# Kernel tuning notes

Hardware: AMD Instinct MI355X
Metric: run time of the kernel (lower is better)

## Reference

```python
import jax, jax.numpy as jnp
import numpy as np

B, SI, ST, D = 2, 1024, 512, 2048
H, KV, HD = 16, 4, 128
E, F, TOPK = 8, 1024, 2
EPS = 1e-6


def _rms(x, w):
    x32 = x.astype(jnp.float32)
    y = x32 * jax.lax.rsqrt(jnp.mean(x32 * x32, axis=-1, keepdims=True) + EPS)
    return y.astype(x.dtype) * w


def _rope(x, cos, sin):
    # x: [B,S,h,HD]; cos/sin: [S,HD//2]. Complex-pair rotation (use_real=False path):
    # pairs (x[2i], x[2i+1]) treated as complex, multiplied by e^{i theta}.
    xr, xi = x[..., 0::2], x[..., 1::2]
    c = cos[None, :, None, :]
    s = sin[None, :, None, :]
    out_r = xr * c - xi * s
    out_i = xr * s + xi * c
    return jnp.stack([out_r, out_i], axis=-1).reshape(x.shape)


def setup_inputs() -> dict:
    key = jax.random.key(0)
    ks = jax.random.split(key, 12)
    def w(k, shape, fan_in):
        return jax.random.normal(k, shape, jnp.float32) * (fan_in ** -0.5)
    pos_i = np.arange(SI)[:, None].astype(np.float32)
    pos_t = np.arange(ST)[:, None].astype(np.float32)
    inv = (1.0 / (10000.0 ** (np.arange(0, HD, 2).astype(np.float32) / HD)))[None, :]
    return {
        'hidden_states': jax.random.normal(ks[0], (B, SI, D), jnp.float32),
        'encoder_hidden_states': jax.random.normal(ks[1], (B, ST, D), jnp.float32),
        'img_cos': jnp.asarray(np.cos(pos_i * inv), jnp.float32),
        'img_sin': jnp.asarray(np.sin(pos_i * inv), jnp.float32),
        'txt_cos': jnp.asarray(np.cos(pos_t * inv), jnp.float32),
        'txt_sin': jnp.asarray(np.sin(pos_t * inv), jnp.float32),
        'norm1_w': jnp.ones((D,), jnp.float32),
        'norm2_w': jnp.ones((D,), jnp.float32),
        'wq': w(ks[2], (D, H * HD), D),
        'wk': w(ks[3], (D, KV * HD), D),
        'wv': w(ks[4], (D, KV * HD), D),
        'wk_txt': w(ks[5], (D, KV * HD), D),
        'wv_txt': w(ks[6], (D, KV * HD), D),
        'wo': w(ks[7], (H * HD, D), H * HD),
        'q_norm_w': jnp.ones((HD,), jnp.float32),
        'k_norm_w': jnp.ones((HD,), jnp.float32),
        'added_k_norm_w': jnp.ones((HD,), jnp.float32),
        'router_w': w(ks[8], (D, E), D),
        'gate_up_proj': w(ks[9], (E, D, 2 * F), D),
        'down_proj': w(ks[10], (E, F, D), F),
    }


def reference(hidden_states, encoder_hidden_states, img_cos, img_sin, txt_cos, txt_sin,
              norm1_w, norm2_w, wq, wk, wv, wk_txt, wv_txt, wo,
              q_norm_w, k_norm_w, added_k_norm_w, router_w, gate_up_proj, down_proj):
    h = hidden_states
    # ---- cross-attn: image queries over concat(image, text) K/V, GQA + RoPE ----
    x = _rms(h, norm1_w)
    q = _rms((x @ wq).reshape(B, SI, H, HD), q_norm_w)
    k_img = _rms((x @ wk).reshape(B, SI, KV, HD), k_norm_w)
    v_img = (x @ wv).reshape(B, SI, KV, HD)
    q = _rope(q, img_cos, img_sin)
    k_img = _rope(k_img, img_cos, img_sin)
    k_txt = _rms((encoder_hidden_states @ wk_txt).reshape(B, ST, KV, HD), added_k_norm_w)
    k_txt = _rope(k_txt, txt_cos, txt_sin)
    v_txt = (encoder_hidden_states @ wv_txt).reshape(B, ST, KV, HD)
    k = jnp.concatenate([k_img, k_txt], axis=1)  # [B, SI+ST, KV, HD]
    v = jnp.concatenate([v_img, v_txt], axis=1)
    k = jnp.repeat(k, H // KV, axis=2)  # GQA repeat_interleave over heads
    v = jnp.repeat(v, H // KV, axis=2)
    scores = jnp.einsum('bqhd,bkhd->bhqk', q, k) * (HD ** -0.5)
    attn = jax.nn.softmax(scores.astype(jnp.float32), axis=-1).astype(q.dtype)
    o = jnp.einsum('bhqk,bkhd->bqhd', attn, v).reshape(B, SI, H * HD)
    h = h + o @ wo
    # ---- MoE: top-k router + packed SwiGLU experts ----
    xt = _rms(h, norm2_w).reshape(B * SI, D)
    probs = jax.nn.softmax((xt @ router_w).astype(jnp.float32), axis=-1)
    topv, topi = jax.lax.top_k(probs, TOPK)
    topv = topv / jnp.sum(topv, axis=-1, keepdims=True)
    wgt = jnp.sum(jax.nn.one_hot(topi, E, dtype=xt.dtype) * topv.astype(xt.dtype)[..., None], axis=1)  # [T,E]
    gate_up = jnp.einsum('td,edg->teg', xt, gate_up_proj)  # [T,E,2F]
    gate, up = gate_up[..., :F], gate_up[..., F:]
    act = jax.nn.silu(gate) * up
    eo = jnp.einsum('tef,efd->ted', act, down_proj)  # [T,E,D]
    moe_out = jnp.einsum('te,ted->td', wgt, eo).reshape(B, SI, D)
    return h + moe_out
```

## Files before the change

kernel.cpp:

```cpp
#include <hip/hip_runtime.h>


typedef __attribute__((ext_vector_type(8))) __bf16 bf16x8;
typedef __attribute__((ext_vector_type(8))) unsigned short u16x8;
typedef __attribute__((ext_vector_type(4))) unsigned short u16x4;
typedef __attribute__((ext_vector_type(4))) float f32x4;

__device__ __forceinline__ unsigned short f2bf(float x) {
  unsigned u = __builtin_bit_cast(unsigned, x);
  u += 0x7fffu + ((u >> 16) & 1u);
  return (unsigned short)(u >> 16);
}
__device__ __forceinline__ float bf2f(unsigned short b) {
  return __builtin_bit_cast(float, ((unsigned)b) << 16);
}

__device__ __forceinline__ void glds16(const unsigned short* g, unsigned short* l) {
  __builtin_amdgcn_global_load_lds(
      (const __attribute__((address_space(1))) void*)g,
      (__attribute__((address_space(3))) void*)l, 16, 0, 0);
}

__device__ __forceinline__ int xcd_swz(int orig, int nwg) {
  int q = nwg >> 3, r = nwg & 7;
  int xcd = orig & 7, idx = orig >> 3;
  int base = (xcd < r) ? xcd * (q + 1) : r * (q + 1) + (xcd - r) * q;
  return base + idx;
}

struct CvtJobs {
  const float* src[8];
  unsigned short* dst[8];
  int K[8];
  int N[8];
  int off[9];
};

__global__ __launch_bounds__(256) void convert_all(CvtJobs jb)
{
  __shared__ unsigned short T[64][66];
  const int bid = blockIdx.x;
  int j = 0;
  #pragma unroll
  for (int i = 0; i < 8; ++i) if (bid >= jb.off[i + 1]) j = i + 1;
  const int local = bid - jb.off[j];
  const int K = jb.K[j], N = jb.N[j];
  const int kb = K >> 6, nb = N >> 6;
  const int kt = local % kb;
  const int rest = local / kb;
  const int nt = rest % nb, zi = rest / nb;
  const float* Wz = jb.src[j] + (size_t)zi * K * N;
  unsigned short* WTz = jb.dst[j] + (size_t)zi * K * N;
  const int k0 = kt * 64, n0 = nt * 64;
  const int tid = threadIdx.x;
  #pragma unroll
  for (int i = tid; i < 64 * 16; i += 256) {
    int k = i >> 4, n4 = (i & 15) * 4;
    float4 v = *(const float4*)&Wz[(size_t)(k0 + k) * N + n0 + n4];
    T[n4 + 0][k] = f2bf(v.x);
    T[n4 + 1][k] = f2bf(v.y);
    T[n4 + 2][k] = f2bf(v.z);
    T[n4 + 3][k] = f2bf(v.w);
  }
  __syncthreads();
  #pragma unroll
  for (int i = tid; i < 64 * 8; i += 256) {
    int n = i >> 3, k8 = (i & 7) * 8;
    *(u16x8*)&WTz[(size_t)(n0 + n) * K + k0 + k8] = *(const u16x8*)&T[n][k8];
  }
}

struct Epi {
  unsigned short* qb;
  unsigned short* kbuf;
  unsigned short* vbuf;
  const float* q_nw;
  const float* k_nw;
  const float* kt_nw;
  const float* icos;
  const float* isin;
  const float* tcos;
  const float* tsin;
  float scale;
};

__global__ __launch_bounds__(256) void gemm_bb(
    const unsigned short* __restrict__ A, const unsigned short* __restrict__ BT,
    float* __restrict__ C, const float* __restrict__ resid,
    int M, int N, int K, int mode, Epi ep)
{
  __shared__ unsigned short As[2][128 * 64];
  __shared__ unsigned short Bs[2][128 * 64];
  const int mb = M >> 7;
  const int w = xcd_swz(blockIdx.x, gridDim.x);
  const int bm = (w % mb) * 128, bn = (w / mb) * 128;
  const int tid = threadIdx.x, lane = tid & 63, wid = tid >> 6;
  const int wm = (wid >> 1) * 64, wn = (wid & 1) * 64;
  const int l16 = lane & 15, g4 = lane >> 4;
  const int rseg = lane >> 3;
  const int csw  = ((lane & 7) ^ rseg) * 8;
  const unsigned short* aSrc[4];
  const unsigned short* bSrc[4];
  #pragma unroll
  for (int p = 0; p < 4; ++p) {
    int row = (p * 4 + wid) * 8 + rseg;
    aSrc[p] = A  + (size_t)(bm + row) * K + csw;
    bSrc[p] = BT + (size_t)(bn + row) * K + csw;
  }
  f32x4 acc[4][4] = {};
  const int NT = K >> 6;
  #pragma unroll
  for (int p = 0; p < 4; ++p) glds16(aSrc[p], &As[0][(p * 4 + wid) * 512]);
  #pragma unroll
  for (int p = 0; p < 4; ++p) glds16(bSrc[p], &Bs[0][(p * 4 + wid) * 512]);
  for (int t = 0; t < NT; ++t) {
    const int cur = t & 1;
    if (t + 1 < NT) {
      const int k0 = (t + 1) << 6;
      #pragma unroll
      for (int p = 0; p < 4; ++p) glds16(aSrc[p] + k0, &As[cur ^ 1][(p * 4 + wid) * 512]);
      #pragma unroll
      for (int p = 0; p < 4; ++p) glds16(bSrc[p] + k0, &Bs[cur ^ 1][(p * 4 + wid) * 512]);
      asm volatile("s_waitcnt vmcnt(8)" ::: "memory");
    } else {
      asm volatile("s_waitcnt vmcnt(0)" ::: "memory");
    }
    __builtin_amdgcn_s_barrier();
    __builtin_amdgcn_sched_barrier(0);
    const unsigned short* ab = &As[cur][0];
    const unsigned short* bb = &Bs[cur][0];
    #pragma unroll
    for (int ks = 0; ks < 2; ++ks) {
      bf16x8 af[4], bf[4];
      #pragma unroll
      for (int i = 0; i < 4; ++i) {
        int ra = wm + i * 16 + l16;
        int rb = wn + i * 16 + l16;
        int ch = ((ks * 4 + g4) ^ (l16 & 7)) * 8;
        af[i] = *(const bf16x8*)&ab[ra * 64 + ch];
        bf[i] = *(const bf16x8*)&bb[rb * 64 + ch];
      }
      #pragma unroll
      for (int mi = 0; mi < 4; ++mi)
        #pragma unroll
        for (int ni = 0; ni < 4; ++ni)
          acc[mi][ni] = __builtin_amdgcn_mfma_f32_16x16x32_bf16(af[mi], bf[ni], acc[mi][ni], 0, 0, 0);
    }
    __builtin_amdgcn_sched_barrier(0);
    __builtin_amdgcn_s_barrier();
  }
  const int r4 = g4 * 4;

  if (mode == 0) {
    #pragma unroll
    for (int mi = 0; mi < 4; ++mi)
      #pragma unroll
      for (int ni = 0; ni < 4; ++ni)
        #pragma unroll
        for (int r = 0; r < 4; ++r) {
          int row = bm + wm + mi * 16 + r4 + r;
          int col = bn + wn + ni * 16 + l16;
          float v = acc[mi][ni][r];
          if (resid) v += resid[(size_t)row * N + col];
          C[(size_t)row * N + col] = v;
        }
    return;
  }

  const int bt = bn >> 7;
  unsigned short* dst;
  const float* nw = nullptr;
  const float* cosT = nullptr;
  const float* sinT = nullptr;
  int h, NH, st, soff, vkind = 0, shift;
  float premul = 1.f;
  int S;
  if (mode == 1) {
    S = 1024; shift = 10;
    if (bt < 16)      { h = bt;      dst = ep.qb;   nw = ep.q_nw; cosT = ep.icos; sinT = ep.isin;
                        NH = 16; st = 1024; soff = 0; premul = ep.scale; }
    else if (bt < 20) { h = bt - 16; dst = ep.kbuf; nw = ep.k_nw; cosT = ep.icos; sinT = ep.isin;
                        NH = 4;  st = 1536; soff = 0; }
    else              { h = bt - 20; dst = ep.vbuf; vkind = 1; NH = 4; st = 1536; soff = 0; }
  } else {
    S = 512; shift = 9;
    if (bt < 4) { h = bt;     dst = ep.kbuf; nw = ep.kt_nw; cosT = ep.tcos; sinT = ep.tsin;
                  NH = 4; st = 1536; soff = 1024; }
    else        { h = bt - 4; dst = ep.vbuf; vkind = 1; NH = 4; st = 1536; soff = 1024; }
  }

  if (vkind) {
    #pragma unroll
    for (int mi = 0; mi < 4; ++mi)
      #pragma unroll
      for (int ni = 0; ni < 4; ++ni)
        #pragma unroll
        for (int r = 0; r < 4; ++r) {
          int row = wm + mi * 16 + r4 + r;
          int d   = wn + ni * 16 + l16;
          int token = bm + row;
          int srow = token & (S - 1), bidx = token >> shift;
          dst[((size_t)(bidx * NH + h) * st + srow + soff) * 128 + d] = f2bf(acc[mi][ni][r]);
        }
    return;
  }

  float* ssb = (float*)&As[0][0];
  float ssp[4][4];
  #pragma unroll
  for (int mi = 0; mi < 4; ++mi)
    #pragma unroll
    for (int r = 0; r < 4; ++r) {
      float v = 0.f;
      #pragma unroll
      for (int ni = 0; ni < 4; ++ni) v += acc[mi][ni][r] * acc[mi][ni][r];
      #pragma unroll
      for (int off = 1; off < 16; off <<= 1) v += __shfl_xor(v, off);
      ssp[mi][r] = v;
    }
  __syncthreads();
  if (l16 == 0) {
    #pragma unroll
    for (int mi = 0; mi < 4; ++mi)
      #pragma unroll
      for (int r = 0; r < 4; ++r)
        ssb[(wid & 1) * 128 + wm + mi * 16 + r4 + r] = ssp[mi][r];
  }
  __syncthreads();
  #pragma unroll
  for (int mi = 0; mi < 4; ++mi)
    #pragma unroll
    for (int r = 0; r < 4; ++r) {
      int row = wm + mi * 16 + r4 + r;
      float tot = ssb[row] + ssb[128 + row];
      float inv = rsqrtf(tot * (1.f / 128.f) + 1e-6f);
      int token = bm + row;
      int srow = token & (S - 1), bidx = token >> shift;
      #pragma unroll
      for (int ni = 0; ni < 4; ++ni) {
        int d = wn + ni * 16 + l16;
        float y = acc[mi][ni][r] * inv * nw[d];
        float part = __shfl_xor(y, 1);
        float c  = cosT[srow * 64 + (d >> 1)];
        float sn = sinT[srow * 64 + (d >> 1)];
        float outv = (d & 1) ? (part * sn + y * c) : (y * c - part * sn);
        dst[((size_t)(bidx * NH + h) * st + srow + soff) * 128 + d] = f2bf(outv * premul);
      }
    }
}

__global__ __launch_bounds__(512, 1) void gemm_moe_256sk(
    const unsigned short* __restrict__ A, const unsigned short* __restrict__ BTall,
    unsigned short* __restrict__ C0, unsigned short* __restrict__ C1,
    const int* __restrict__ counts, const int* __restrict__ offsets,
    const int* __restrict__ pair_token, const unsigned short* __restrict__ zbuf,
    int gather, int K, int N)
{
  const int w = xcd_swz(blockIdx.x, gridDim.x);
  const int e = w >> 7;
  const int local = w & 127;
  const int bm = ((local >> 4) & 7) * 256;
  const int kh = (local >> 3) & 1;
  const int bn = (local & 7) * 256;
  const int cnt = counts[e];
  if (bm >= cnt) return;
  const int base = offsets[e];
  const int Kh = K >> 1;
  unsigned short* __restrict__ C = kh ? C1 : C0;
  __shared__ unsigned short As[2][256 * 64];
  __shared__ unsigned short Bs[2][256 * 64];
  __shared__ int rowmap[256];
  const int tid = threadIdx.x, lane = tid & 63, wid = tid >> 6;
  const int wr = wid >> 2, wc = wid & 3;
  const int l16 = lane & 15, g4 = lane >> 4;
  const int rseg = lane >> 3;
  const int csw  = ((lane & 7) ^ rseg) * 8;
  if (tid < 256) {
    int lr = bm + tid;
    rowmap[tid] = (lr < cnt) ? (gather ? pair_token[base + lr] : base + lr) : -1;
  }
  __syncthreads();
  const unsigned short* BT = BTall + (size_t)e * N * K;
  const unsigned short* aSrc[4];
  const unsigned short* bSrc[4];
  int aOk[4];
  #pragma unroll
  for (int p = 0; p < 4; ++p) {
    int row = (p * 8 + wid) * 8 + rseg;
    int tok = rowmap[row];
    aOk[p] = (tok >= 0);
    aSrc[p] = aOk[p] ? (A + (size_t)tok * K + kh * Kh + csw) : (zbuf + csw);
    bSrc[p] = BT + (size_t)(bn + row) * K + kh * Kh + csw;
  }
  f32x4 acc[8][4] = {};
  const int NT = Kh >> 6;
  #pragma unroll
  for (int p = 0; p < 4; ++p) glds16(aSrc[p], &As[0][(p * 8 + wid) * 512]);
  #pragma unroll
  for (int p = 0; p < 4; ++p) glds16(bSrc[p], &Bs[0][(p * 8 + wid) * 512]);
  for (int t = 0; t < NT; ++t) {
    const int cur = t & 1;
    if (t + 1 < NT) {
      const int k0 = (t + 1) << 6;
      #pragma unroll
      for (int p = 0; p < 4; ++p)
        glds16(aSrc[p] + (aOk[p] ? k0 : 0), &As[cur ^ 1][(p * 8 + wid) * 512]);
      #pragma unroll
      for (int p = 0; p < 4; ++p)
        glds16(bSrc[p] + k0, &Bs[cur ^ 1][(p * 8 + wid) * 512]);
      asm volatile("s_waitcnt vmcnt(8)" ::: "memory");
    } else {
      asm volatile("s_waitcnt vmcnt(0)" ::: "memory");
    }
    __builtin_amdgcn_s_barrier();
    __builtin_amdgcn_sched_barrier(0);
    const unsigned short* ab = &As[cur][0];
    const unsigned short* bb = &Bs[cur][0];
    #pragma unroll
    for (int ks = 0; ks < 2; ++ks) {
      const int ch = ((ks * 4 + g4) ^ (l16 & 7)) * 8;
      bf16x8 bf[4];
      #pragma unroll
      for (int j = 0; j < 4; ++j)
        bf[j] = *(const bf16x8*)&bb[(wc * 64 + j * 16 + l16) * 64 + ch];
      #pragma unroll
      for (int mi = 0; mi < 8; ++mi) {
        bf16x8 af = *(const bf16x8*)&ab[(wr * 128 + mi * 16 + l16) * 64 + ch];
        #pragma unroll
        for (int ni = 0; ni < 4; ++ni)
          acc[mi][ni] = __builtin_amdgcn_mfma_f32_16x16x32_bf16(af, bf[ni], acc[mi][ni], 0, 0, 0);
      }
    }
    __builtin_amdgcn_sched_barrier(0);
    __builtin_amdgcn_s_barrier();
  }
  const int r4 = g4 * 4;
  #pragma unroll
  for (int mi = 0; mi < 8; ++mi)
    #pragma unroll
    for (int ni = 0; ni < 4; ++ni)
      #pragma unroll
      for (int r = 0; r < 4; ++r) {
        int lrow = bm + wr * 128 + mi * 16 + r4 + r;
        int col  = bn + wc * 64 + ni * 16 + l16;
        if (lrow < cnt)
          C[(size_t)(base + lrow) * N + col] = f2bf(acc[mi][ni][r]);
      }
}

__global__ __launch_bounds__(256) void pre_norm(
    const float* __restrict__ hidden, const float* __restrict__ w,
    unsigned short* __restrict__ x_bf,
    const float* __restrict__ enc, unsigned short* __restrict__ enc_bf)
{
  const int row = blockIdx.x;
  const int tid = threadIdx.x;
  if (row >= 2048) {
    const int r = row - 2048;
    const float* x = enc + (size_t)r * 2048 + tid * 8;
    unsigned short* o = enc_bf + (size_t)r * 2048 + tid * 8;
    float4 a = *(const float4*)&x[0];
    float4 b = *(const float4*)&x[4];
    o[0] = f2bf(a.x); o[1] = f2bf(a.y); o[2] = f2bf(a.z); o[3] = f2bf(a.w);
    o[4] = f2bf(b.x); o[5] = f2bf(b.y); o[6] = f2bf(b.z); o[7] = f2bf(b.w);
    return;
  }
  const float* x = hidden + (size_t)row * 2048;
  float4 a = *(const float4*)&x[tid * 8];
  float4 b = *(const float4*)&x[tid * 8 + 4];
  float s = a.x*a.x + a.y*a.y + a.z*a.z + a.w*a.w
          + b.x*b.x + b.y*b.y + b.z*b.z + b.w*b.w;
  #pragma unroll
  for (int off = 1; off < 64; off <<= 1) s += __shfl_xor(s, off);
  __shared__ float red[4];
  if ((tid & 63) == 0) red[tid >> 6] = s;
  __syncthreads();
  float inv = rsqrtf((red[0] + red[1] + red[2] + red[3]) * (1.f / 2048.f) + 1e-6f);
  float4 wa = *(const float4*)&w[tid * 8];
  float4 wb = *(const float4*)&w[tid * 8 + 4];
  unsigned short* o = x_bf + (size_t)row * 2048 + tid * 8;
  o[0] = f2bf(a.x * inv * wa.x); o[1] = f2bf(a.y * inv * wa.y);
  o[2] = f2bf(a.z * inv * wa.z); o[3] = f2bf(a.w * inv * wa.w);
  o[4] = f2bf(b.x * inv * wb.x); o[5] = f2bf(b.y * inv * wb.y);
  o[6] = f2bf(b.z * inv * wb.z); o[7] = f2bf(b.w * inv * wb.w);
}

__global__ __launch_bounds__(256) void rmsnorm_router(
    const float* __restrict__ in, const float* __restrict__ w,
    unsigned short* __restrict__ xt, const float* __restrict__ rw,
    int* __restrict__ topi, float* __restrict__ topw, int* __restrict__ counts)
{
  const int row = blockIdx.x;
  const int tid = threadIdx.x, lane = tid & 63, wid = tid >> 6;
  const float* x = in + (size_t)row * 2048;
  float4 a = *(const float4*)&x[tid * 8];
  float4 b = *(const float4*)&x[tid * 8 + 4];
  float s = a.x*a.x + a.y*a.y + a.z*a.z + a.w*a.w
          + b.x*b.x + b.y*b.y + b.z*b.z + b.w*b.w;
  #pragma unroll
  for (int off = 1; off < 64; off <<= 1) s += __shfl_xor(s, off);
  __shared__ float red[4];
  __shared__ float rl[4][8];
  if (lane == 0) red[wid] = s;
  __syncthreads();
  float inv = rsqrtf((red[0] + red[1] + red[2] + red[3]) * (1.f / 2048.f) + 1e-6f);
  float4 wa = *(const float4*)&w[tid * 8];
  float4 wb = *(const float4*)&w[tid * 8 + 4];
  float y[8] = {a.x * inv * wa.x, a.y * inv * wa.y, a.z * inv * wa.z, a.w * inv * wa.w,
                b.x * inv * wb.x, b.y * inv * wb.y, b.z * inv * wb.z, b.w * inv * wb.w};
  unsigned short* o = xt + (size_t)row * 2048 + tid * 8;
  #pragma unroll
  for (int j = 0; j < 8; ++j) o[j] = f2bf(y[j]);
  float lg[8] = {};
  #pragma unroll
  for (int j = 0; j < 8; ++j) {
    int d = tid * 8 + j;
    const float4 r0 = *(const float4*)&rw[d * 8];
    const float4 r1 = *(const float4*)&rw[d * 8 + 4];
    lg[0] += y[j] * r0.x; lg[1] += y[j] * r0.y; lg[2] += y[j] * r0.z; lg[3] += y[j] * r0.w;
    lg[4] += y[j] * r1.x; lg[5] += y[j] * r1.y; lg[6] += y[j] * r1.z; lg[7] += y[j] * r1.w;
  }
  #pragma unroll
  for (int e = 0; e < 8; ++e)
    #pragma unroll
    for (int off = 1; off < 64; off <<= 1) lg[e] += __shfl_xor(lg[e], off);
  if (lane == 0) {
    #pragma unroll
    for (int e = 0; e < 8; ++e) rl[wid][e] = lg[e];
  }
  __syncthreads();
  if (tid == 0) {
    float l[8];
    #pragma unroll
    for (int e = 0; e < 8; ++e) l[e] = rl[0][e] + rl[1][e] + rl[2][e] + rl[3][e];
    float v0 = l[0]; int e0 = 0;
    #pragma unroll
    for (int e = 1; e < 8; ++e) if (l[e] > v0) { v0 = l[e]; e0 = e; }
    float v1 = -1e30f; int e1 = 0;
    #pragma unroll
    for (int e = 0; e < 8; ++e) if (e != e0 && l[e] > v1) { v1 = l[e]; e1 = e; }
    float x1 = expf(v1 - v0);
    float w0 = 1.f / (1.f + x1);
    float w1 = x1 / (1.f + x1);
    topi[2 * row] = e0; topi[2 * row + 1] = e1;
    topw[2 * row] = w0; topw[2 * row + 1] = w1;
    atomicAdd(&counts[e0], 1);
    atomicAdd(&counts[e1], 1);
  }
}

__global__ __launch_bounds__(256) void route_build(
    const int* __restrict__ counts, int* __restrict__ offsets,
    const int* __restrict__ topi,
    int* __restrict__ pair_token, int* __restrict__ token_slot)
{
  __shared__ int soff[9];
  __shared__ int sfill[8];
  const int tid = threadIdx.x;
  if (tid == 0) {
    int a = 0;
    #pragma unroll
    for (int e = 0; e < 8; ++e) { soff[e] = a; a += counts[e]; }
    soff[8] = a;
  }
  if (tid < 8) sfill[tid] = 0;
  __syncthreads();
  if (tid < 9) offsets[tid] = soff[tid];
  for (int t = tid; t < 2048; t += 256) {
    #pragma unroll
    for (int k = 0; k < 2; ++k) {
      int e = topi[2 * t + k];
      int slot = soff[e] + atomicAdd(&sfill[e], 1);
      pair_token[slot] = t;
      token_slot[2 * t + k] = slot;
    }
  }
}

__global__ __launch_bounds__(512) void attn_kernel(
    const unsigned short* __restrict__ q,
    const unsigned short* __restrict__ kbuf,
    const unsigned short* __restrict__ vbuf,
    unsigned short* __restrict__ o)
{
  const int SK = 1536;
  const int w = xcd_swz(blockIdx.x, gridDim.x);
  const int bh = w >> 3;
  const int b = bh >> 4, h = bh & 15, kvh = h >> 2;
  const int q0 = (w & 7) * 128;
  const int tid = threadIdx.x, lane = tid & 63, wid = tid >> 6;
  const int l16 = lane & 15, kb = (lane >> 4) * 8, r4 = (lane >> 4) * 4;
  __shared__ unsigned short KsL[64 * 128];
  __shared__ unsigned short VTL[128 * 64];
  __shared__ unsigned short PsL[8 * 16 * 64];
  const int sr0 = tid >> 4;
  const int scc = (tid & 15) * 8;

  const unsigned short* qrow =
      q + ((size_t)(b * 16 + h) * 1024 + q0 + wid * 16 + l16) * 128;
  bf16x8 qf[4];
  #pragma unroll
  for (int ks = 0; ks < 4; ++ks) qf[ks] = *(const bf16x8*)&qrow[ks * 32 + kb];
  float mrow[4] = {-1e30f, -1e30f, -1e30f, -1e30f};
  float lrow[4] = {0.f, 0.f, 0.f, 0.f};
  f32x4 oacc[8] = {};
  const unsigned short* kb_base = kbuf + (size_t)(b * 4 + kvh) * SK * 128;
  const unsigned short* vb_base = vbuf + (size_t)(b * 4 + kvh) * SK * 128;

  u16x8 k0[2], v0[2], k1[2], v1[2];

#define ATT_LOAD(kr, vr, kt1)                                                 \
  {                                                                           \
    _Pragma("unroll")                                                         \
    for (int i = 0; i < 2; ++i) {                                             \
      kr[i] = *(const u16x8*)&kb_base[(size_t)((kt1) + sr0 + 32 * i) * 128 + scc]; \
      vr[i] = *(const u16x8*)&vb_base[(size_t)((kt1) + sr0 + 32 * i) * 128 + scc]; \
    }                                                                         \
  }

#define ATT_STAGE(kr, vr)                                                     \
  {                                                                           \
    _Pragma("unroll")                                                         \
    for (int i = 0; i < 2; ++i) {                                             \
      int rr = sr0 + 32 * i;                                                  \
      *(u16x8*)&KsL[rr * 128 + (((scc >> 3) ^ (rr & 7)) << 3)] = kr[i];       \
      _Pragma("unroll")                                                       \
      for (int j = 0; j < 8; ++j)                                             \
        VTL[(scc + j) * 64 + ((((rr >> 3) ^ ((scc + j) >> 3)) & 7) << 3) + (rr & 7)] = vr[i][j]; \
    }                                                                         \
  }

  auto compute = [&]() {
    f32x4 sacc[4] = {};
    __builtin_amdgcn_s_setprio(1);
    #pragma unroll
    for (int ks = 0; ks < 4; ++ks) {
      #pragma unroll
      for (int ni = 0; ni < 4; ++ni) {
        int rr = ni * 16 + l16;
        bf16x8 kf = *(const bf16x8*)
            &KsL[rr * 128 + ((((ks * 32 + kb) >> 3) ^ (rr & 7)) << 3)];
        sacc[ni] = __builtin_amdgcn_mfma_f32_16x16x32_bf16(qf[ks], kf, sacc[ni], 0, 0, 0);
      }
    }
    __builtin_amdgcn_s_setprio(0);
    float pv[4][4], alpha[4];
    #pragma unroll
    for (int r = 0; r < 4; ++r) {
      float tm = fmaxf(fmaxf(sacc[0][r], sacc[1][r]), fmaxf(sacc[2][r], sacc[3][r]));
      #pragma unroll
      for (int off = 1; off < 16; off <<= 1) tm = fmaxf(tm, __shfl_xor(tm, off));
      float mn = fmaxf(mrow[r], tm);
      alpha[r] = __expf(mrow[r] - mn);
      float s = 0.f;
      #pragma unroll
      for (int ni = 0; ni < 4; ++ni) {
        float p = __expf(sacc[ni][r] - mn);
        pv[ni][r] = p; s += p;
      }
      #pragma unroll
      for (int off = 1; off < 16; off <<= 1) s += __shfl_xor(s, off);
      lrow[r] = lrow[r] * alpha[r] + s;
      mrow[r] = mn;
    }
    #pragma unroll
    for (int ni = 0; ni < 8; ++ni)
      #pragma unroll
      for (int r = 0; r < 4; ++r) oacc[ni][r] *= alpha[r];
    #pragma unroll
    for (int ni = 0; ni < 4; ++ni)
      #pragma unroll
      for (int r = 0; r < 4; ++r) {
        int row = r4 + r, col = ni * 16 + l16;
        PsL[wid * 1024 + row * 64 + ((((col >> 3) ^ (row & 7)) & 7) << 3) + (col & 7)]
            = f2bf(pv[ni][r]);
      }
    asm volatile("s_waitcnt lgkmcnt(0)" ::: "memory");
    __builtin_amdgcn_sched_barrier(0);
    __builtin_amdgcn_s_setprio(1);
    #pragma unroll
    for (int ks = 0; ks < 2; ++ks) {
      bf16x8 pf = *(const bf16x8*)
          &PsL[wid * 1024 + l16 * 64 + ((((ks * 32 + kb) >> 3) ^ (l16 & 7)) << 3)];
      #pragma unroll
      for (int ni = 0; ni < 8; ++ni) {
        int d = ni * 16 + l16;
        bf16x8 vf = *(const bf16x8*)
            &VTL[d * 64 + ((((ks * 32 + kb) >> 3) ^ ((d >> 3) & 7)) << 3)];
        oacc[ni] = __builtin_amdgcn_mfma_f32_16x16x32_bf16(pf, vf, oacc[ni], 0, 0, 0);
      }
    }
    __builtin_amdgcn_s_setprio(0);
  };

  ATT_LOAD(k0, v0, 0);
  for (int t = 0; t < 24; t += 2) {
    ATT_STAGE(k0, v0);
    ATT_LOAD(k1, v1, (t + 1) * 64);
    asm volatile("s_waitcnt lgkmcnt(0)" ::: "memory");
    __builtin_amdgcn_s_barrier();
    __builtin_amdgcn_sched_barrier(0);
    compute();
    __builtin_amdgcn_sched_barrier(0);
    __builtin_amdgcn_s_barrier();
    ATT_STAGE(k1, v1);
    if (t + 2 < 24) ATT_LOAD(k0, v0, (t + 2) * 64);
    asm volatile("s_waitcnt lgkmcnt(0)" ::: "memory");
    __builtin_amdgcn_s_barrier();
    __builtin_amdgcn_sched_barrier(0);
    compute();
    __builtin_amdgcn_sched_barrier(0);
    __builtin_amdgcn_s_barrier();
  }
#undef ATT_LOAD
#undef ATT_STAGE

  #pragma unroll
  for (int ni = 0; ni < 8; ++ni)
    #pragma unroll
    for (int r = 0; r < 4; ++r) {
      float val = oacc[ni][r] / lrow[r];
      size_t row = (size_t)b * 1024 + q0 + wid * 16 + r4 + r;
      o[row * 2048 + h * 128 + ni * 16 + l16] = f2bf(val);
    }
}

__global__ __launch_bounds__(256) void act_silu2(
    const unsigned short* __restrict__ gu0, const unsigned short* __restrict__ gu1,
    unsigned short* __restrict__ act)
{
  int p = blockIdx.x;
  int c = threadIdx.x * 4;
  u16x4 g0 = *(const u16x4*)&gu0[(size_t)p * 2048 + c];
  u16x4 g1 = *(const u16x4*)&gu1[(size_t)p * 2048 + c];
  u16x4 u0 = *(const u16x4*)&gu0[(size_t)p * 2048 + 1024 + c];
  u16x4 u1 = *(const u16x4*)&gu1[(size_t)p * 2048 + 1024 + c];
  #pragma unroll
  for (int j = 0; j < 4; ++j) {
    float g = bf2f(g0[j]) + bf2f(g1[j]);
    float u = bf2f(u0[j]) + bf2f(u1[j]);
    float a = g / (1.f + __expf(-g)) * u;
    act[(size_t)p * 1024 + c + j] = f2bf(a);
  }
}

__global__ __launch_bounds__(256) void moe_combine2(
    float* __restrict__ out, const unsigned short* __restrict__ eo0,
    const unsigned short* __restrict__ eo1,
    const int* __restrict__ token_slot, const float* __restrict__ topw)
{
  int t = blockIdx.x;
  int c = threadIdx.x * 8;
  int s0 = token_slot[2 * t], s1 = token_slot[2 * t + 1];
  float w0 = topw[2 * t], w1 = topw[2 * t + 1];
  u16x8 a0 = *(const u16x8*)&eo0[(size_t)s0 * 2048 + c];
  u16x8 a1 = *(const u16x8*)&eo1[(size_t)s0 * 2048 + c];
  u16x8 b0 = *(const u16x8*)&eo0[(size_t)s1 * 2048 + c];
  u16x8 b1 = *(const u16x8*)&eo1[(size_t)s1 * 2048 + c];
  #pragma unroll
  for (int j0 = 0; j0 < 8; j0 += 4) {
    float4 v = *(const float4*)&out[(size_t)t * 2048 + c + j0];
    v.x += w0 * (bf2f(a0[j0+0]) + bf2f(a1[j0+0])) + w1 * (bf2f(b0[j0+0]) + bf2f(b1[j0+0]));
    v.y += w0 * (bf2f(a0[j0+1]) + bf2f(a1[j0+1])) + w1 * (bf2f(b0[j0+1]) + bf2f(b1[j0+1]));
    v.z += w0 * (bf2f(a0[j0+2]) + bf2f(a1[j0+2])) + w1 * (bf2f(b0[j0+2]) + bf2f(b1[j0+2]));
    v.w += w0 * (bf2f(a0[j0+3]) + bf2f(a1[j0+3])) + w1 * (bf2f(b0[j0+3]) + bf2f(b1[j0+3]));
    *(float4*)&out[(size_t)t * 2048 + c + j0] = v;
  }
}

extern "C" void kernel_launch(void* const* d_in, const int* in_sizes, int n_in,
                              void* d_out, int out_size, void* d_ws, size_t ws_size,
                              hipStream_t stream)
{
  const float* hidden  = (const float*)d_in[0];
  const float* enc     = (const float*)d_in[1];
  const float* img_cos = (const float*)d_in[2];
  const float* img_sin = (const float*)d_in[3];
  const float* txt_cos = (const float*)d_in[4];
  const float* txt_sin = (const float*)d_in[5];
  const float* norm1_w = (const float*)d_in[6];
  const float* norm2_w = (const float*)d_in[7];
  const float* wq      = (const float*)d_in[8];
  const float* wk      = (const float*)d_in[9];
  const float* wv      = (const float*)d_in[10];
  const float* wk_txt  = (const float*)d_in[11];
  const float* wv_txt  = (const float*)d_in[12];
  const float* wo      = (const float*)d_in[13];
  const float* q_norm_w       = (const float*)d_in[14];
  const float* k_norm_w       = (const float*)d_in[15];
  const float* added_k_norm_w = (const float*)d_in[16];
  const float* router_w       = (const float*)d_in[17];
  const float* gate_up_proj   = (const float*)d_in[18];
  const float* down_proj      = (const float*)d_in[19];
  float* out = (float*)d_out;

  char* ws = (char*)d_ws;
  size_t off = 0;
  auto alloc = [&](size_t bytes) {
    void* p = ws + off;
    off += (bytes + 255) & ~(size_t)255;
    return p;
  };
  unsigned short* wqkvT  = (unsigned short*)alloc(3072ULL * 2048 * 2);
  unsigned short* wkvtT  = (unsigned short*)alloc(1024ULL * 2048 * 2);
  unsigned short* woT    = (unsigned short*)alloc(2048ULL * 2048 * 2);
  unsigned short* gupT   = (unsigned short*)alloc(8ULL * 2048 * 2048 * 2);
  unsigned short* dnT    = (unsigned short*)alloc(8ULL * 2048 * 1024 * 2);
  unsigned short* x_bf   = (unsigned short*)alloc(2048ULL * 2048 * 2);
  unsigned short* enc_bf = (unsigned short*)alloc(1024ULL * 2048 * 2);
  unsigned short* gu0 = (unsigned short*)alloc(4096ULL * 2048 * 2);
  unsigned short* gu1 = (unsigned short*)alloc(4096ULL * 2048 * 2);
  unsigned short* qb   = (unsigned short*)alloc(2048ULL * 2048 * 2);
  unsigned short* kbuf = (unsigned short*)alloc(2ULL * 4 * 1536 * 128 * 2);
  unsigned short* vbuf = (unsigned short*)alloc(2ULL * 4 * 1536 * 128 * 2);
  unsigned short* obuf = (unsigned short*)alloc(2048ULL * 2048 * 2);
  unsigned short* act  = obuf;
  unsigned short* xt   = (unsigned short*)alloc(2048ULL * 2048 * 2);
  int*   ctrl  = (int*)alloc(64 * sizeof(int));
  int*   topi  = (int*)alloc(4096 * 4);
  float* topw  = (float*)alloc(4096 * 4);
  int*   tslot = (int*)alloc(4096 * 4);
  int*   ptok  = (int*)alloc(4096 * 4);
  unsigned short* zbuf = (unsigned short*)alloc(256);
  int* counts = ctrl, * offsets = ctrl + 16;

  hipMemsetAsync(ctrl, 0, 64, stream);
  hipMemsetAsync(zbuf, 0, 256, stream);

  const float scale = 0.08838834764831845f;

  CvtJobs jb;
  jb.src[0] = wq;     jb.dst[0] = wqkvT;                  jb.K[0] = 2048; jb.N[0] = 2048;
  jb.src[1] = wk;     jb.dst[1] = wqkvT + 2048ULL * 2048; jb.K[1] = 2048; jb.N[1] = 512;
  jb.src[2] = wv;     jb.dst[2] = wqkvT + 2560ULL * 2048; jb.K[2] = 2048; jb.N[2] = 512;
  jb.src[3] = wk_txt; jb.dst[3] = wkvtT;                  jb.K[3] = 2048; jb.N[3] = 512;
  jb.src[4] = wv_txt; jb.dst[4] = wkvtT + 512ULL * 2048;  jb.K[4] = 2048; jb.N[4] = 512;
  jb.src[5] = wo;     jb.dst[5] = woT;                    jb.K[5] = 2048; jb.N[5] = 2048;
  jb.src[6] = gate_up_proj; jb.dst[6] = gupT;             jb.K[6] = 2048; jb.N[6] = 2048;
  jb.src[7] = down_proj;    jb.dst[7] = dnT;              jb.K[7] = 1024; jb.N[7] = 2048;
  jb.off[0] = 0;     jb.off[1] = 1024;  jb.off[2] = 1280; jb.off[3] = 1536;
  jb.off[4] = 1792;  jb.off[5] = 2048;  jb.off[6] = 3072; jb.off[7] = 11264;
  jb.off[8] = 15360;
  convert_all<<<15360, 256, 0, stream>>>(jb);

  pre_norm<<<3072, 256, 0, stream>>>(hidden, norm1_w, x_bf, enc, enc_bf);

  Epi ep;
  ep.qb = qb; ep.kbuf = kbuf; ep.vbuf = vbuf;
  ep.q_nw = q_norm_w; ep.k_nw = k_norm_w; ep.kt_nw = added_k_norm_w;
  ep.icos = img_cos; ep.isin = img_sin; ep.tcos = txt_cos; ep.tsin = txt_sin;
  ep.scale = scale;

  gemm_bb<<<384, 256, 0, stream>>>(x_bf, wqkvT, nullptr, nullptr, 2048, 3072, 2048, 1, ep);
  gemm_bb<<<64, 256, 0, stream>>>(enc_bf, wkvtT, nullptr, nullptr, 1024, 1024, 2048, 2, ep);

  attn_kernel<<<256, 512, 0, stream>>>(qb, kbuf, vbuf, obuf);

  gemm_bb<<<256, 256, 0, stream>>>(obuf, woT, out, hidden, 2048, 2048, 2048, 0, ep);

  rmsnorm_router<<<2048, 256, 0, stream>>>(out, norm2_w, xt, router_w,
                                           topi, topw, counts);
  route_build<<<1, 256, 0, stream>>>(counts, offsets, topi, ptok, tslot);

  gemm_moe_256sk<<<1024, 512, 0, stream>>>(xt, gupT, gu0, gu1,
                                           counts, offsets, ptok, zbuf, 1, 2048, 2048);
  act_silu2<<<4096, 256, 0, stream>>>(gu0, gu1, act);
  gemm_moe_256sk<<<1024, 512, 0, stream>>>(act, dnT, gu0, gu1,
                                           counts, offsets, ptok, zbuf, 0, 1024, 2048);
  moe_combine2<<<2048, 256, 0, stream>>>(out, gu0, gu1, tslot, topw);
}
```

Before: 512.7 us.

## Fold large weight conversions into the attention launch as extra blocks

The single weight-conversion kernel is split in two. The small QKV/text KV conversions still run first because the projections need them. The wo, gate_up and down conversions become extra blocks appended to the attention grid, so the memory-bound transpose/cast runs alongside the compute-bound attention on otherwise idle CU capacity instead of as its own serial launch. The cost is a shared 48KB LDS allocation for every block, including the convert blocks, which limits how many fit per CU, and possible bandwidth contention with attention.

```diff
diff --git a/kernel.cpp b/kernel.cpp
--- a/kernel.cpp
+++ b/kernel.cpp
@@ -36,7 +36,7 @@
   int off[9];
 };
 
-__global__ __launch_bounds__(256) void convert_all(CvtJobs jb)
+__global__ __launch_bounds__(256) void convert_small(CvtJobs jb)
 {
   __shared__ unsigned short T[64][66];
   const int bid = blockIdx.x;
@@ -477,22 +477,59 @@
   }
 }
 
-__global__ __launch_bounds__(512) void attn_kernel(
+__global__ __launch_bounds__(512) void attn_plus_convert(
     const unsigned short* __restrict__ q,
     const unsigned short* __restrict__ kbuf,
     const unsigned short* __restrict__ vbuf,
-    unsigned short* __restrict__ o)
-{
+    unsigned short* __restrict__ o,
+    CvtJobs jb)
+{
+  __shared__ unsigned short SMEM[24576];
+  const int tid = threadIdx.x;
+
+  if (blockIdx.x >= 256) {
+    unsigned short (*T)[66] = (unsigned short(*)[66])SMEM;
+    const int bid = blockIdx.x - 256;
+    int j = 0;
+    #pragma unroll
+    for (int i = 0; i < 8; ++i) if (bid >= jb.off[i + 1]) j = i + 1;
+    const int local = bid - jb.off[j];
+    const int K = jb.K[j], N = jb.N[j];
+    const int kb2 = K >> 6, nb = N >> 6;
+    const int kt = local % kb2;
+    const int rest = local / kb2;
+    const int nt = rest % nb, zi = rest / nb;
+    const float* Wz = jb.src[j] + (size_t)zi * K * N;
+    unsigned short* WTz = jb.dst[j] + (size_t)zi * K * N;
+    const int k0 = kt * 64, n0 = nt * 64;
+    #pragma unroll
+    for (int i = tid; i < 64 * 16; i += 512) {
+      int k = i >> 4, n4 = (i & 15) * 4;
+      float4 v = *(const float4*)&Wz[(size_t)(k0 + k) * N + n0 + n4];
+      T[n4 + 0][k] = f2bf(v.x);
+      T[n4 + 1][k] = f2bf(v.y);
+      T[n4 + 2][k] = f2bf(v.z);
+      T[n4 + 3][k] = f2bf(v.w);
+    }
+    __syncthreads();
+    {
+      int i = tid;
+      int n = i >> 3, k8 = (i & 7) * 8;
+      *(u16x8*)&WTz[(size_t)(n0 + n) * K + k0 + k8] = *(const u16x8*)&T[n][k8];
+    }
+    return;
+  }
+
+  unsigned short* KsL = SMEM;
+  unsigned short* VTL = SMEM + 8192;
+  unsigned short* PsL = SMEM + 16384;
   const int SK = 1536;
-  const int w = xcd_swz(blockIdx.x, gridDim.x);
+  const int w = xcd_swz(blockIdx.x, 256);
   const int bh = w >> 3;
   const int b = bh >> 4, h = bh & 15, kvh = h >> 2;
   const int q0 = (w & 7) * 128;
-  const int tid = threadIdx.x, lane = tid & 63, wid = tid >> 6;
+  const int lane = tid & 63, wid = tid >> 6;
   const int l16 = lane & 15, kb = (lane >> 4) * 8, r4 = (lane >> 4) * 4;
-  __shared__ unsigned short KsL[64 * 128];
-  __shared__ unsigned short VTL[128 * 64];
-  __shared__ unsigned short PsL[8 * 16 * 64];
   const int sr0 = tid >> 4;
   const int scc = (tid & 15) * 8;
 
@@ -525,8 +562,8 @@
       int rr = sr0 + 32 * i;                                                  \
       *(u16x8*)&KsL[rr * 128 + (((scc >> 3) ^ (rr & 7)) << 3)] = kr[i];       \
       _Pragma("unroll")                                                       \
-      for (int j = 0; j < 8; ++j)                                             \
-        VTL[(scc + j) * 64 + ((((rr >> 3) ^ ((scc + j) >> 3)) & 7) << 3) + (rr & 7)] = vr[i][j]; \
+      for (int jj = 0; jj < 8; ++jj)                                          \
+        VTL[(scc + jj) * 64 + ((((rr >> 3) ^ ((scc + jj) >> 3)) & 7) << 3) + (rr & 7)] = vr[i][jj]; \
     }                                                                         \
   }
 
@@ -729,19 +766,19 @@
 
   const float scale = 0.08838834764831845f;
 
-  CvtJobs jb;
-  jb.src[0] = wq;     jb.dst[0] = wqkvT;                  jb.K[0] = 2048; jb.N[0] = 2048;
-  jb.src[1] = wk;     jb.dst[1] = wqkvT + 2048ULL * 2048; jb.K[1] = 2048; jb.N[1] = 512;
-  jb.src[2] = wv;     jb.dst[2] = wqkvT + 2560ULL * 2048; jb.K[2] = 2048; jb.N[2] = 512;
-  jb.src[3] = wk_txt; jb.dst[3] = wkvtT;                  jb.K[3] = 2048; jb.N[3] = 512;
-  jb.src[4] = wv_txt; jb.dst[4] = wkvtT + 512ULL * 2048;  jb.K[4] = 2048; jb.N[4] = 512;
-  jb.src[5] = wo;     jb.dst[5] = woT;                    jb.K[5] = 2048; jb.N[5] = 2048;
-  jb.src[6] = gate_up_proj; jb.dst[6] = gupT;             jb.K[6] = 2048; jb.N[6] = 2048;
-  jb.src[7] = down_proj;    jb.dst[7] = dnT;              jb.K[7] = 1024; jb.N[7] = 2048;
-  jb.off[0] = 0;     jb.off[1] = 1024;  jb.off[2] = 1280; jb.off[3] = 1536;
-  jb.off[4] = 1792;  jb.off[5] = 2048;  jb.off[6] = 3072; jb.off[7] = 11264;
-  jb.off[8] = 15360;
-  convert_all<<<15360, 256, 0, stream>>>(jb);
+  CvtJobs jb1;
+  jb1.src[0] = wq;     jb1.dst[0] = wqkvT;                  jb1.K[0] = 2048; jb1.N[0] = 2048;
+  jb1.src[1] = wk;     jb1.dst[1] = wqkvT + 2048ULL * 2048; jb1.K[1] = 2048; jb1.N[1] = 512;
+  jb1.src[2] = wv;     jb1.dst[2] = wqkvT + 2560ULL * 2048; jb1.K[2] = 2048; jb1.N[2] = 512;
+  jb1.src[3] = wk_txt; jb1.dst[3] = wkvtT;                  jb1.K[3] = 2048; jb1.N[3] = 512;
+  jb1.src[4] = wv_txt; jb1.dst[4] = wkvtT + 512ULL * 2048;  jb1.K[4] = 2048; jb1.N[4] = 512;
+  jb1.src[5] = wv_txt; jb1.dst[5] = wkvtT + 512ULL * 2048;  jb1.K[5] = 2048; jb1.N[5] = 512;
+  jb1.src[6] = jb1.src[5]; jb1.dst[6] = jb1.dst[5]; jb1.K[6] = 2048; jb1.N[6] = 512;
+  jb1.src[7] = jb1.src[5]; jb1.dst[7] = jb1.dst[5]; jb1.K[7] = 2048; jb1.N[7] = 512;
+  jb1.off[0] = 0;    jb1.off[1] = 1024; jb1.off[2] = 1280; jb1.off[3] = 1536;
+  jb1.off[4] = 1792; jb1.off[5] = 2048; jb1.off[6] = 2048; jb1.off[7] = 2048;
+  jb1.off[8] = 2048;
+  convert_small<<<2048, 256, 0, stream>>>(jb1);
 
   pre_norm<<<3072, 256, 0, stream>>>(hidden, norm1_w, x_bf, enc, enc_bf);
 
@@ -754,7 +791,15 @@
   gemm_bb<<<384, 256, 0, stream>>>(x_bf, wqkvT, nullptr, nullptr, 2048, 3072, 2048, 1, ep);
   gemm_bb<<<64, 256, 0, stream>>>(enc_bf, wkvtT, nullptr, nullptr, 1024, 1024, 2048, 2, ep);
 
-  attn_kernel<<<256, 512, 0, stream>>>(qb, kbuf, vbuf, obuf);
+  CvtJobs jb2;
+  jb2.src[0] = wo;           jb2.dst[0] = woT;  jb2.K[0] = 2048; jb2.N[0] = 2048;
+  jb2.src[1] = gate_up_proj; jb2.dst[1] = gupT; jb2.K[1] = 2048; jb2.N[1] = 2048;
+  jb2.src[2] = down_proj;    jb2.dst[2] = dnT;  jb2.K[2] = 1024; jb2.N[2] = 2048;
+  for (int i = 3; i < 8; ++i) { jb2.src[i] = wo; jb2.dst[i] = woT; jb2.K[i] = 2048; jb2.N[i] = 2048; }
+  jb2.off[0] = 0;     jb2.off[1] = 1024;  jb2.off[2] = 9216;  jb2.off[3] = 13312;
+  jb2.off[4] = 13312; jb2.off[5] = 13312; jb2.off[6] = 13312; jb2.off[7] = 13312;
+  jb2.off[8] = 13312;
+  attn_plus_convert<<<256 + 13312, 512, 0, stream>>>(qb, kbuf, vbuf, obuf, jb2);
 
   gemm_bb<<<256, 256, 0, stream>>>(obuf, woT, out, hidden, 2048, 2048, 2048, 0, ep);
 
```

New measurement: 568.5 us. 10.9% more time.
